# Kernel tuning notes

Hardware: AMD Instinct MI355X
Metric: run time of the kernel (lower is better)

## Reference

```python
import jax, jax.numpy as jnp
import numpy as np

RATIO = 0.5  # SAGPooling ratio


def setup_inputs() -> dict:
    key = jax.random.key(0)
    ks = jax.random.split(key, 6)
    B, n, d, out_dim, Eg = 128, 512, 256, 256, 4096  # graphs, nodes/graph, feat, proj out, edges/graph
    N = B * n
    x = jax.random.normal(ks[0], (N, d), dtype=jnp.float32)
    # edges connect nodes within the same graph (contiguous node blocks)
    src = jax.random.randint(ks[1], (B, Eg), 0, n)
    dst = jax.random.randint(ks[2], (B, Eg), 0, n)
    off = (jnp.arange(B) * n)[:, None]
    edge_index = jnp.stack([(src + off).reshape(-1), (dst + off).reshape(-1)]).astype(jnp.int32)
    batch = jnp.repeat(jnp.arange(B), n).astype(jnp.int32)
    s = 1.0 / np.sqrt(d).astype(np.float32)
    w_rel = jax.random.normal(ks[3], (d, 1), dtype=jnp.float32) * s   # GraphConv lin_rel (has bias)
    b_rel = jnp.zeros((1,), dtype=jnp.float32)
    w_root = jax.random.normal(ks[4], (d, 1), dtype=jnp.float32) * s  # GraphConv lin_root (no bias)
    w_proj = jax.random.normal(ks[5], (d, out_dim), dtype=jnp.float32) * s  # projection Linear
    b_proj = jnp.zeros((out_dim,), dtype=jnp.float32)
    return {"x": x, "edge_index": edge_index, "batch": batch, "num_graphs": B,
            "w_rel": w_rel, "b_rel": b_rel, "w_root": w_root,
            "w_proj": w_proj, "b_proj": b_proj}


def reference(x, edge_index, batch, num_graphs, w_rel, b_rel, w_root, w_proj, b_proj):
    N, d = x.shape
    n = N // num_graphs                    # equal-size graphs
    k = int(np.ceil(RATIO * n))            # PyG topk: ceil(ratio * num_nodes)
    src, dst = edge_index[0], edge_index[1]
    # GraphConv(node_dim, 1): score_i = lin_rel(sum_{j->i} x_j) + lin_root(x_i)
    agg = jax.ops.segment_sum(x[src], dst, num_segments=N)          # [N, d]
    score = jnp.tanh((agg @ w_rel + b_rel + x @ w_root)[:, 0])       # [N], tanh nonlinearity
    sb = score.reshape(num_graphs, n)                                # [B, n]
    top_vals, top_idx = jax.lax.top_k(sb, k)                         # per-graph topk
    xb = x.reshape(num_graphs, n, d)
    x_sel = jnp.take_along_axis(xb, top_idx[:, :, None], axis=1)     # [B, k, d]
    x_sel = x_sel * top_vals[:, :, None]                             # x[perm] * score[perm] (multiplier=1)
    pooled = x_sel.mean(axis=1)                                      # global_mean_pool over k kept nodes
    return pooled @ w_proj + b_proj                                  # [B, out_dim]
```

## Files before the change

### kernel.cpp

```cpp
#include <hip/hip_runtime.h>

#define D        256
#define NPG      512
#define BG       128
#define KSEL     256
#define EPG      4096
#define NN       (BG * NPG)
#define ET       (BG * EPG)

__global__ __launch_bounds__(256) void k_proj_scores(
        const float* __restrict__ x,
        const float* __restrict__ w_rel, const float* __restrict__ w_root,
        float* __restrict__ p, float* __restrict__ r,
        float* __restrict__ pooled) {
    int tid  = threadIdx.x;
    int wave = tid >> 6, lane = tid & 63;
    int node = blockIdx.x * 4 + wave;

    if (blockIdx.x < BG) pooled[(size_t)blockIdx.x * D + tid] = 0.f;

    const float4* x4  = (const float4*)(x + (size_t)node * D);
    float4 xv = x4[lane];
    float4 wr = ((const float4*)w_rel)[lane];
    float4 wo = ((const float4*)w_root)[lane];
    float pv = xv.x * wr.x + xv.y * wr.y + xv.z * wr.z + xv.w * wr.w;
    float rv = xv.x * wo.x + xv.y * wo.y + xv.z * wo.z + xv.w * wo.w;
    #pragma unroll
    for (int off = 32; off; off >>= 1) {
        pv += __shfl_xor(pv, off, 64);
        rv += __shfl_xor(rv, off, 64);
    }
    if (lane == 0) { p[node] = pv; r[node] = rv; }
}

__global__ __launch_bounds__(512) void k_score_select(
        const int* __restrict__ ei,
        const float* __restrict__ p, const float* __restrict__ r,
        const float* __restrict__ b_rel,
        int* __restrict__ sel_idx, float* __restrict__ sel_val) {
    __shared__ float s_p[NPG];
    __shared__ float s_agg[NPG];
    __shared__ float s_val[NPG];
    __shared__ int   s_cnt;
    int b = blockIdx.x, tid = threadIdx.x;
    int base = b * NPG;

    s_p[tid]   = p[base + tid];
    s_agg[tid] = 0.f;
    if (tid == 0) s_cnt = 0;
    __syncthreads();

    const int* src = ei + (size_t)b * EPG;
    const int* dst = ei + ET + (size_t)b * EPG;
    #pragma unroll
    for (int e = tid; e < EPG; e += 512)
        atomicAdd(&s_agg[dst[e] - base], s_p[src[e] - base]);
    __syncthreads();

    float sv = tanhf(s_agg[tid] + b_rel[0] + r[base + tid]);
    s_val[tid] = sv;
    __syncthreads();

    int cnt = 0;
    #pragma unroll 8
    for (int i = 0; i < NPG; ++i) {
        float o = s_val[i];
        cnt += (o > sv) || (o == sv && i < tid);
    }
    if (cnt < KSEL) {
        int pos = atomicAdd(&s_cnt, 1);
        sel_idx[b * KSEL + pos] = base + tid;
        sel_val[b * KSEL + pos] = sv;
    }
}

__global__ __launch_bounds__(256) void k_pool(
        const float* __restrict__ x,
        const int* __restrict__ sel_idx, const float* __restrict__ sel_val,
        float* __restrict__ pooled) {
    __shared__ int   s_i[16];
    __shared__ float s_v[16];
    int b = blockIdx.x, q = blockIdx.y, tid = threadIdx.x;
    if (tid < 16) {
        s_i[tid] = sel_idx[b * KSEL + q * 16 + tid];
        s_v[tid] = sel_val[b * KSEL + q * 16 + tid];
    }
    __syncthreads();
    float acc = 0.f;
    #pragma unroll
    for (int m = 0; m < 16; ++m)
        acc += s_v[m] * x[(size_t)s_i[m] * D + tid];
    atomicAdd(&pooled[b * D + tid], acc);
}

__global__ __launch_bounds__(256) void k_out(
        const float* __restrict__ pooled,
        const float* __restrict__ w_proj, const float* __restrict__ b_proj,
        float* __restrict__ out) {
    __shared__ float s_p[D];
    int b = blockIdx.x, tid = threadIdx.x;
    s_p[tid] = pooled[(size_t)b * D + tid] * (1.0f / KSEL);
    __syncthreads();
    float acc = b_proj[tid];
    #pragma unroll 8
    for (int kk = 0; kk < D; ++kk)
        acc += s_p[kk] * w_proj[kk * D + tid];
    out[(size_t)b * D + tid] = acc;
}

extern "C" void kernel_launch(void* const* d_in, const int* in_sizes, int n_in,
                              void* d_out, int out_size, void* d_ws, size_t ws_size,
                              hipStream_t stream) {
    const float* x      = (const float*)d_in[0];
    const int*   ei     = (const int*)d_in[1];
    const float* w_rel  = (const float*)d_in[4];
    const float* b_rel  = (const float*)d_in[5];
    const float* w_root = (const float*)d_in[6];
    const float* w_proj = (const float*)d_in[7];
    const float* b_proj = (const float*)d_in[8];
    float* out = (float*)d_out;

    float* p       = (float*)d_ws;
    float* r       = p + NN;
    float* pooled  = r + NN;
    float* sel_val = pooled + (size_t)BG * D;
    int*   sel_idx = (int*)(sel_val + (size_t)BG * KSEL);

    k_proj_scores<<<NN / 4, 256, 0, stream>>>(x, w_rel, w_root, p, r, pooled);
    k_score_select<<<BG, 512, 0, stream>>>(ei, p, r, b_rel, sel_idx, sel_val);
    k_pool<<<dim3(BG, 16), 256, 0, stream>>>(x, sel_idx, sel_val, pooled);
    k_out<<<BG, 256, 0, stream>>>(pooled, w_proj, b_proj, out);
}
```

Baseline: 145.7 us.

## Fuse pooling with output projection via last-block counter, split rank count across 1024 threads

Merges the pool and output-projection kernels into one launch. Each graph's eight pool blocks increment a per-graph counter, and the last block to arrive computes the projection, which removes one kernel launch. The selection kernel now uses 1024 threads so each node's rank count over 512 scores is split in two halves of 256 and then summed, halving the serial loop length. Pool blocks now handle 32 selected rows each instead of 16. The counter requires a threadfence, an atomic read-back and a final serialized block per graph.

```diff
diff --git a/kernel.cpp b/kernel.cpp
--- a/kernel.cpp
+++ b/kernel.cpp
@@ -12,15 +12,15 @@
         const float* __restrict__ x,
         const float* __restrict__ w_rel, const float* __restrict__ w_root,
         float* __restrict__ p, float* __restrict__ r,
-        float* __restrict__ pooled) {
+        float* __restrict__ pooled, int* __restrict__ cnt) {
     int tid  = threadIdx.x;
     int wave = tid >> 6, lane = tid & 63;
     int node = blockIdx.x * 4 + wave;
 
-    if (blockIdx.x < BG) pooled[(size_t)blockIdx.x * D + tid] = 0.f;
+    if (blockIdx.x < BG) pooled[blockIdx.x * D + tid] = 0.f;
+    if (blockIdx.x == 0 && tid < BG) cnt[tid] = 0;
 
-    const float4* x4  = (const float4*)(x + (size_t)node * D);
-    float4 xv = x4[lane];
+    float4 xv = ((const float4*)(x + (size_t)node * D))[lane];
     float4 wr = ((const float4*)w_rel)[lane];
     float4 wo = ((const float4*)w_root)[lane];
     float pv = xv.x * wr.x + xv.y * wr.y + xv.z * wr.z + xv.w * wr.w;
@@ -33,7 +33,7 @@
     if (lane == 0) { p[node] = pv; r[node] = rv; }
 }
 
-__global__ __launch_bounds__(512) void k_score_select(
+__global__ __launch_bounds__(1024) void k_score_select(
         const int* __restrict__ ei,
         const float* __restrict__ p, const float* __restrict__ r,
         const float* __restrict__ b_rel,
@@ -41,71 +41,88 @@
     __shared__ float s_p[NPG];
     __shared__ float s_agg[NPG];
     __shared__ float s_val[NPG];
+    __shared__ int   s_cnt2[1024];
     __shared__ int   s_cnt;
     int b = blockIdx.x, tid = threadIdx.x;
     int base = b * NPG;
 
-    s_p[tid]   = p[base + tid];
-    s_agg[tid] = 0.f;
+    if (tid < NPG) { s_p[tid] = p[base + tid]; s_agg[tid] = 0.f; }
     if (tid == 0) s_cnt = 0;
     __syncthreads();
 
     const int* src = ei + (size_t)b * EPG;
     const int* dst = ei + ET + (size_t)b * EPG;
     #pragma unroll
-    for (int e = tid; e < EPG; e += 512)
+    for (int q = 0; q < 4; ++q) {
+        int e = tid + q * 1024;
         atomicAdd(&s_agg[dst[e] - base], s_p[src[e] - base]);
+    }
     __syncthreads();
 
-    float sv = tanhf(s_agg[tid] + b_rel[0] + r[base + tid]);
-    s_val[tid] = sv;
+    if (tid < NPG)
+        s_val[tid] = tanhf(s_agg[tid] + b_rel[0] + r[base + tid]);
     __syncthreads();
 
-    int cnt = 0;
-    #pragma unroll 8
-    for (int i = 0; i < NPG; ++i) {
-        float o = s_val[i];
-        cnt += (o > sv) || (o == sv && i < tid);
+    {
+        int j = tid & (NPG - 1);
+        int half = tid >> 9;
+        float sv = s_val[j];
+        int lo = half * 256, c = 0;
+        #pragma unroll 8
+        for (int i = lo; i < lo + 256; ++i) {
+            float o = s_val[i];
+            c += (o > sv) || (o == sv && i < j);
+        }
+        s_cnt2[tid] = c;
     }
-    if (cnt < KSEL) {
-        int pos = atomicAdd(&s_cnt, 1);
-        sel_idx[b * KSEL + pos] = base + tid;
-        sel_val[b * KSEL + pos] = sv;
+    __syncthreads();
+    if (tid < NPG) {
+        int rank = s_cnt2[tid] + s_cnt2[tid + NPG];
+        if (rank < KSEL) {
+            int pos = atomicAdd(&s_cnt, 1);
+            sel_idx[b * KSEL + pos] = base + tid;
+            sel_val[b * KSEL + pos] = s_val[tid];
+        }
     }
 }
 
-__global__ __launch_bounds__(256) void k_pool(
+__global__ __launch_bounds__(256) void k_pool_out(
         const float* __restrict__ x,
         const int* __restrict__ sel_idx, const float* __restrict__ sel_val,
-        float* __restrict__ pooled) {
-    __shared__ int   s_i[16];
-    __shared__ float s_v[16];
+        float* __restrict__ pooled, int* __restrict__ cnt,
+        const float* __restrict__ w_proj, const float* __restrict__ b_proj,
+        float* __restrict__ out) {
+    __shared__ int   s_i[32];
+    __shared__ float s_v[32];
+    __shared__ float s_pool[D];
+    __shared__ int   s_win;
     int b = blockIdx.x, q = blockIdx.y, tid = threadIdx.x;
-    if (tid < 16) {
-        s_i[tid] = sel_idx[b * KSEL + q * 16 + tid];
-        s_v[tid] = sel_val[b * KSEL + q * 16 + tid];
+
+    if (tid < 32) {
+        s_i[tid] = sel_idx[b * KSEL + q * 32 + tid];
+        s_v[tid] = sel_val[b * KSEL + q * 32 + tid];
     }
     __syncthreads();
+
     float acc = 0.f;
-    #pragma unroll
-    for (int m = 0; m < 16; ++m)
+    #pragma unroll 8
+    for (int m = 0; m < 32; ++m)
         acc += s_v[m] * x[(size_t)s_i[m] * D + tid];
     atomicAdd(&pooled[b * D + tid], acc);
-}
+    __threadfence();
+    __syncthreads();
+    if (tid == 0) s_win = atomicAdd(&cnt[b], 1);
+    __syncthreads();
 
-__global__ __launch_bounds__(256) void k_out(
-        const float* __restrict__ pooled,
-        const float* __restrict__ w_proj, const float* __restrict__ b_proj,
-        float* __restrict__ out) {
-    __shared__ float s_p[D];
-    int b = blockIdx.x, tid = threadIdx.x;
-    s_p[tid] = pooled[(size_t)b * D + tid] * (1.0f / KSEL);
-    __syncthreads();
-    float acc = b_proj[tid];
-    #pragma unroll 8
-    for (int kk = 0; kk < D; ++kk)
-        acc += s_p[kk] * w_proj[kk * D + tid];
-    out[(size_t)b * D + tid] = acc;
+    if (s_win == 7) {
+        s_pool[tid] = atomicAdd(&pooled[b * D + tid], 0.0f) * (1.0f / KSEL);
+        __syncthreads();
+        float o = b_proj[tid];
+        #pragma unroll 8
+        for (int kk = 0; kk < D; ++kk)
+            o += s_pool[kk] * w_proj[kk * D + tid];
+        out[(size_t)b * D + tid] = o;
+    }
 }
 
 extern "C" void kernel_launch(void* const* d_in, const int* in_sizes, int n_in,
@@ -122,12 +139,13 @@
 
     float* p       = (float*)d_ws;
     float* r       = p + NN;
-    float* pooled  = r + NN;
-    float* sel_val = pooled + (size_t)BG * D;
+    float* sel_val = r + NN;
     int*   sel_idx = (int*)(sel_val + (size_t)BG * KSEL);
+    float* pooled  = (float*)(sel_idx + (size_t)BG * KSEL);
+    int*   cnt     = (int*)(pooled + (size_t)BG * D);
 
-    k_proj_scores<<<NN / 4, 256, 0, stream>>>(x, w_rel, w_root, p, r, pooled);
-    k_score_select<<<BG, 512, 0, stream>>>(ei, p, r, b_rel, sel_idx, sel_val);
-    k_pool<<<dim3(BG, 16), 256, 0, stream>>>(x, sel_idx, sel_val, pooled);
-    k_out<<<BG, 256, 0, stream>>>(pooled, w_proj, b_proj, out);
+    k_proj_scores<<<NN / 4, 256, 0, stream>>>(x, w_rel, w_root, p, r, pooled, cnt);
+    k_score_select<<<BG, 1024, 0, stream>>>(ei, p, r, b_rel, sel_idx, sel_val);
+    k_pool_out<<<dim3(BG, 8), 256, 0, stream>>>(x, sel_idx, sel_val, pooled, cnt,
+                                                w_proj, b_proj, out);
 }
```

Result: slower. 206.0 us (+41.4%).
